# Optimization experiments

Hardware: AMD Instinct MI355X
Metric: run time of the kernel (lower is better)

Reference implementation:

```python
import jax, jax.numpy as jnp
import numpy as np

B, N, F_IN = 32, 512, 64
HEADS = (8, 8)
HIDS = (64, 64)
EDGE_P = 0.05  # graph density
NEG_SLOPE = 0.2
NEG_INF = -1e20


def setup_inputs() -> dict:
    key = jax.random.key(0)
    ks = jax.random.split(key, 8)
    x = jax.random.normal(ks[0], (B, N, F_IN), dtype=jnp.float32)
    adj = (jax.random.uniform(ks[1], (B, N, N)) < EDGE_P).astype(jnp.float32)
    adj = jnp.maximum(adj, adj.transpose(0, 2, 1))  # symmetric adjacency
    # mask = (batch, row): every (b, n) pair gets the masked softmax
    b_idx = jnp.repeat(jnp.arange(B, dtype=jnp.int32), N)   # [B*N]
    r_idx = jnp.tile(jnp.arange(N, dtype=jnp.int32), B)     # [B*N]
    # layer 0: f_in=64 -> f_out=64, H=8 ; layer 1: f_in=64*8=512 -> f_out=64, H=8
    W0 = jax.random.normal(ks[2], (F_IN, HIDS[0]), dtype=jnp.float32) / jnp.sqrt(jnp.float32(F_IN))
    a_src0 = jax.random.normal(ks[3], (HIDS[0], HEADS[0]), dtype=jnp.float32) / jnp.sqrt(jnp.float32(HIDS[0]))
    a_dst0 = jax.random.normal(ks[4], (HIDS[0], HEADS[0]), dtype=jnp.float32) / jnp.sqrt(jnp.float32(HIDS[0]))
    f_in1 = HIDS[0] * HEADS[0]
    W1 = jax.random.normal(ks[5], (f_in1, HIDS[1]), dtype=jnp.float32) / jnp.sqrt(jnp.float32(f_in1))
    a_src1 = jax.random.normal(ks[6], (HIDS[1], HEADS[1]), dtype=jnp.float32) / jnp.sqrt(jnp.float32(HIDS[1]))
    a_dst1 = jax.random.normal(ks[7], (HIDS[1], HEADS[1]), dtype=jnp.float32) / jnp.sqrt(jnp.float32(HIDS[1]))
    return dict(x=x, adj=adj, b_idx=b_idx, r_idx=r_idx,
                W0=W0, a_src0=a_src0, a_dst0=a_dst0,
                W1=W1, a_src1=a_src1, a_dst1=a_dst1)


def _gat_layer(x, adj, b_idx, r_idx, W, a_src, a_dst):
    # x: [B,N,f_in], adj: [B,N,N] (diag already set), W: [f_in,F], a_*: [F,H]
    hp = x @ W                                        # [B,N,F]
    s = jnp.einsum('bnf,fh->bhn', hp, a_src)          # attn_src
    d = jnp.einsum('bnf,fh->bhn', hp, a_dst)          # attn_dst
    attn = s[:, :, :, None] + d[:, :, None, :]        # [B,H,N,N]
    attn = jnp.where(attn >= 0, attn, NEG_SLOPE * attn)  # leaky_relu(0.2)
    attn = jnp.where(adj[:, None, :, :] == 0, 0.0, attn)  # masked_fill(adj==0, 0)
    rows = attn[b_idx, :, r_idx, :]                   # [K,H,N]
    rows = jnp.where(rows == 0.0, NEG_INF, rows)
    rows = jax.nn.softmax(rows, axis=-1)
    attn = attn.at[b_idx, :, r_idx, :].set(rows)
    return jnp.einsum('bhij,bjf->bhif', attn, hp)     # [B,H,N,F]


def reference(x, adj, b_idx, r_idx, W0, a_src0, a_dst0, W1, a_src1, a_dst1):
    Bn, Nn = x.shape[:2]
    # torch mutates adj in place: adj[batch,row,row] = 1 (self loops)
    adj = adj.at[b_idx, r_idx, r_idx].set(1.0)
    o = _gat_layer(x, adj, b_idx, r_idx, W0, a_src0, a_dst0)      # [B,H,N,F0]
    x1 = jax.nn.elu(o.transpose(0, 2, 1, 3).reshape(Bn, Nn, -1))  # [B,N,H*F0]
    o2 = _gat_layer(x1, adj, b_idx, r_idx, W1, a_src1, a_dst1)    # [B,H,N,F1]
    return o2.mean(axis=1)                                        # [B,N,F1]
```

## Files before the change

### kernel.cpp

```cpp
#include <hip/hip_runtime.h>
#include <hip/hip_bf16.h>
#include <math.h>

#define BB 32
#define NN 512

typedef _Float16 f16x8 __attribute__((ext_vector_type(8)));
typedef __fp16  fp16x2 __attribute__((ext_vector_type(2)));
typedef float f32x4 __attribute__((ext_vector_type(4)));

#define MFMA16(a, b, c) __builtin_amdgcn_mfma_f32_16x16x32_f16(a, b, c, 0, 0, 0)

union AF { f16x8 v; unsigned int u[4]; };

__device__ __forceinline__ void gload_lds16(const void* g, void* l) {
    __builtin_amdgcn_global_load_lds(
        (const __attribute__((address_space(1))) unsigned int*)g,
        (__attribute__((address_space(3))) unsigned int*)l, 16, 0, 0);
}

__global__ __launch_bounds__(256) void k_wt_prep(
    const float* __restrict__ W0, _Float16* __restrict__ W0T,
    const float* __restrict__ W1, _Float16* __restrict__ W1T)
{
    int id = blockIdx.x * 256 + threadIdx.x;
    const float* W; _Float16* WT; int KT, task;
    if (id < 512) { W = W0; WT = W0T; KT = 64;  task = id; }
    else          { W = W1; WT = W1T; KT = 512; task = id - 512; }
    int n = task & 63, gabs = task >> 6;
    int c = gabs >> 3, g = gabs & 7;
    f16x8 hv;
#pragma unroll
    for (int e = 0; e < 8; ++e)
        hv[e] = (_Float16)W[(size_t)(gabs * 8 + e) * 64 + n];
    *(f16x8*)(WT + (size_t)n * KT + c * 64 + (g ^ (n & 7)) * 8) = hv;
}

__global__ __launch_bounds__(256) void k_maxd(
    const float* __restrict__ dTg, float* __restrict__ maxd,
    float* __restrict__ E, float* __restrict__ Eb)
{
    __shared__ float sm[4];
    int bh = blockIdx.x;
    int t = threadIdx.x, lane = t & 63, w = t >> 6;
    const float* p = dTg + (size_t)bh * NN;
    float d0 = p[t], d1 = p[t + 256];
    float m = fmaxf(d0, d1);
#pragma unroll
    for (int off = 32; off; off >>= 1) m = fmaxf(m, __shfl_xor(m, off));
    if (lane == 0) sm[w] = m;
    __syncthreads();
    float mx = fmaxf(fmaxf(sm[0], sm[1]), fmaxf(sm[2], sm[3]));
    if (t == 0) maxd[bh] = mx;
    float* Ep  = E  + (size_t)bh * NN;
    float* Ebp = Eb + (size_t)bh * NN;
    Ep[t]        = __expf(d0 - mx);
    Ep[t + 256]  = __expf(d1 - mx);
    Ebp[t]       = __expf(0.2f * (d0 - mx));
    Ebp[t + 256] = __expf(0.2f * (d1 - mx));
}

static __device__ __forceinline__ void epi_sd_hpt(
    const float* ctile, const float* asd_f, int row0, int t,
    float* __restrict__ s, float* __restrict__ dTg, _Float16* __restrict__ hpT)
{
    int b = row0 >> 9, jb = row0 & 511;
    if (t < 128) {
        int rr = t >> 3, h = t & 7;
        float sv = 0.f, dv = 0.f;
#pragma unroll
        for (int f = 0; f < 64; ++f) {
            float hv = ctile[rr * 66 + f];
            sv = fmaf(hv, asd_f[f * 8 + h], sv);
            dv = fmaf(hv, asd_f[512 + f * 8 + h], dv);
        }
        s[((size_t)b * NN + jb + rr) * 8 + h] = sv;
        dTg[((size_t)b * 8 + h) * NN + jb + rr] = dv;
    } else {
        int t2 = t - 128;
        int f = t2 >> 1, jl = (t2 & 1) * 8;
        f16x8 hv;
#pragma unroll
        for (int e = 0; e < 8; ++e)
            hv[e] = (_Float16)ctile[(jl + e) * 66 + f];
        *(f16x8*)(hpT + ((size_t)b * 64 + f) * NN + jb + jl) = hv;
    }
}

__global__ __launch_bounds__(256) void k_gemm0(
    const float* __restrict__ x, const _Float16* __restrict__ W0T,
    const float* __restrict__ a_src, const float* __restrict__ a_dst,
    const float* __restrict__ adj, unsigned long long* __restrict__ adjb,
    float* __restrict__ s, float* __restrict__ dTg, _Float16* __restrict__ hpT)
{
    __shared__ float ctile[16 * 66];
    __shared__ float asd_f[1024];
    int t = threadIdx.x, row0 = blockIdx.x * 16;
    int lane = t & 63, w = t >> 6, cn = lane & 15, rq = lane >> 4;

    ((float4*)asd_f)[t] = (t < 128) ? ((const float4*)a_src)[t]
                                    : ((const float4*)a_dst)[t - 128];
    f32x4 acc;
#pragma unroll
    for (int e = 0; e < 4; ++e) acc[e] = 0.f;
#pragma unroll
    for (int ks = 0; ks < 2; ++ks) {
        const float* xp = x + (size_t)(row0 + cn) * 64 + ks * 32 + rq * 8;
        float4 x0 = *(const float4*)xp, x1 = *(const float4*)(xp + 4);
        f16x8 ah = {(_Float16)x0.x, (_Float16)x0.y, (_Float16)x0.z, (_Float16)x0.w,
                    (_Float16)x1.x, (_Float16)x1.y, (_Float16)x1.z, (_Float16)x1.w};
        int nn = w * 16 + cn;
        f16x8 bh = *(const f16x8*)(W0T + (size_t)nn * 64 + (((ks * 4 + rq) ^ (nn & 7)) * 8));
        acc = MFMA16(ah, bh, acc);
    }
#pragma unroll
    for (int r = 0; r < 4; ++r)
        ctile[(rq * 4 + r) * 66 + w * 16 + cn] = acc[r];
    __syncthreads();
    epi_sd_hpt(ctile, asd_f, row0, t, s, dTg, hpT);

#pragma unroll
    for (int rl = 0; rl < 4; ++rl) {
        int gi = row0 + w * 4 + rl;
        int i = gi & (NN - 1);
        const float* ap = adj + (size_t)gi * NN;
#pragma unroll
        for (int jc8 = 0; jc8 < 8; ++jc8) {
            float v = ap[jc8 * 64 + lane];
            unsigned long long m = __ballot((v != 0.f) || (jc8 * 64 + lane == i));
            if (lane == 0) adjb[(size_t)gi * 8 + jc8] = m;
        }
    }
}

template<int MODE>
__global__ __launch_bounds__(256, 4) void k_attn_fused(
    const unsigned long long* __restrict__ adjb, const float* __restrict__ s,
    const float* __restrict__ dTg, const float* __restrict__ maxd,
    const float* __restrict__ E, const float* __restrict__ Eb,
    const _Float16* __restrict__ hpT,
    const _Float16* __restrict__ W1T,
    const float* __restrict__ a_src, const float* __restrict__ a_dst,
    float* __restrict__ s_out, float* __restrict__ dTg_out,
    _Float16* __restrict__ hpT_out, float* __restrict__ o_f)
{
    __shared__ __align__(16) char smem[32768];
    _Float16* hTd0 = (_Float16*)smem;
    _Float16* hTd1 = (_Float16*)(smem + 8192);

    int blk = blockIdx.x;
    int vb = ((blk & 7) << 7) | (blk >> 3);
    int b = vb >> 5, i0 = (vb & 31) << 4;
    int row0 = vb * 16;
    int t = threadIdx.x, lane = t & 63, w = t >> 6;
    int cn = lane & 15, rq = lane >> 4;
    int h0 = 2 * w, h1 = h0 + 1;
    int myrow = i0 + cn;

    const _Float16* hb = hpT + (size_t)b * 64 * NN;

    int f0 = t >> 3, g0 = t & 7;
    const _Float16* src0 = hb + (size_t)f0 * NN + ((g0 ^ (f0 & 7)) * 8);
    const _Float16* src1 = hb + (size_t)(f0 + 32) * NN + ((g0 ^ (f0 & 7)) * 8);
    {
        _Float16* db = hTd0 + (w << 9);
        gload_lds16(src0, db);
        gload_lds16(src1, db + 2048);
    }

    float sv0 = s[((size_t)b * NN + myrow) * 8 + h0];
    float sv1 = s[((size_t)b * NN + myrow) * 8 + h1];
    float md0 = maxd[b * 8 + h0], md1 = maxd[b * 8 + h1];
    float M0 = fmaxf(sv0 + md0, 0.f);
    float M1 = fmaxf(sv1 + md1, 0.f);
    float c00 = __expf(sv0 + md0 - M0), cb0 = __expf(0.2f * (sv0 + md0) - M0);
    float c01 = __expf(sv1 + md1 - M1), cb1 = __expf(0.2f * (sv1 + md1) - M1);

    const float* dg0  = dTg + ((size_t)b * 8 + h0) * NN;
    const float* dg1  = dTg + ((size_t)b * 8 + h1) * NN;
    const float* Er0  = E   + ((size_t)b * 8 + h0) * NN;
    const float* Er1  = E   + ((size_t)b * 8 + h1) * NN;
    const float* Ebr0 = Eb  + ((size_t)b * 8 + h0) * NN;
    const float* Ebr1 = Eb  + ((size_t)b * 8 + h1) * NN;
    const unsigned long long* abr = adjb + ((size_t)b * NN + myrow) * 8;
    int rq8 = rq * 8;

    f16x8 ones;
#pragma unroll
    for (int e = 0; e < 8; ++e) ones[e] = (_Float16)1.0f;

    f32x4 acc[2][4], accrs[2];
#pragma unroll
    for (int hh = 0; hh < 2; ++hh) {
#pragma unroll
        for (int e = 0; e < 4; ++e) accrs[hh][e] = 0.f;
#pragma unroll
        for (int ft = 0; ft < 4; ++ft)
#pragma unroll
            for (int e = 0; e < 4; ++e) acc[hh][ft][e] = 0.f;
    }

    unsigned long long mb = abr[0];
    __syncthreads();

#pragma unroll 2
    for (int jcx = 0; jcx < 8; ++jcx) {
        int jc = jcx * 64;
        const _Float16* hTc = (jcx & 1) ? hTd1 : hTd0;
        if (jcx < 7) {
            _Float16* db = ((jcx & 1) ? hTd0 : hTd1) + (w << 9);
            gload_lds16(src0 + jc + 64, db);
            gload_lds16(src1 + jc + 64, db + 2048);
        }
        unsigned long long mbn = (jcx < 7) ? abr[jcx + 1] : 0ull;
        unsigned int ml = (unsigned int)mb, mhh = (unsigned int)(mb >> 32);
#pragma unroll
        for (int ks = 0; ks < 2; ++ks) {
            int j0 = jc + ks * 32 + rq8;
            unsigned int mby = ((ks ? mhh : ml) >> rq8) & 0xffu;
            float dd0[8], dd1[8], Ev0[8], Ev1[8], Eb0v[8], Eb1v[8];
            *(float4*)&dd0[0]  = *(const float4*)(dg0 + j0);
            *(float4*)&dd0[4]  = *(const float4*)(dg0 + j0 + 4);
            *(float4*)&dd1[0]  = *(const float4*)(dg1 + j0);
            *(float4*)&dd1[4]  = *(const float4*)(dg1 + j0 + 4);
            *(float4*)&Ev0[0]  = *(const float4*)(Er0 + j0);
            *(float4*)&Ev0[4]  = *(const float4*)(Er0 + j0 + 4);
            *(float4*)&Ev1[0]  = *(const float4*)(Er1 + j0);
            *(float4*)&Ev1[4]  = *(const float4*)(Er1 + j0 + 4);
            *(float4*)&Eb0v[0] = *(const float4*)(Ebr0 + j0);
            *(float4*)&Eb0v[4] = *(const float4*)(Ebr0 + j0 + 4);
            *(float4*)&Eb1v[0] = *(const float4*)(Ebr1 + j0);
            *(float4*)&Eb1v[4] = *(const float4*)(Ebr1 + j0 + 4);
            AF aA, aB;
#pragma unroll
            for (int e = 0; e < 8; e += 2) {
                float pA[2], pB[2];
#pragma unroll
                for (int q = 0; q < 2; ++q) {
                    int ee = e + q;
                    bool con = (mby >> ee) & 1u;
                    float e0 = sv0 + dd0[ee];
                    float p0 = (e0 >= 0.f) ? c00 * Ev0[ee] : cb0 * Eb0v[ee];
                    pA[q] = (con && e0 != 0.f) ? p0 : 0.f;
                    float e1 = sv1 + dd1[ee];
                    float p1 = (e1 >= 0.f) ? c01 * Ev1[ee] : cb1 * Eb1v[ee];
                    pB[q] = (con && e1 != 0.f) ? p1 : 0.f;
                }
                fp16x2 ka = __builtin_amdgcn_cvt_pkrtz(pA[0], pA[1]);
                fp16x2 kb = __builtin_amdgcn_cvt_pkrtz(pB[0], pB[1]);
                aA.u[e >> 1] = __builtin_bit_cast(unsigned int, ka);
                aB.u[e >> 1] = __builtin_bit_cast(unsigned int, kb);
            }
            accrs[0] = MFMA16(aA.v, ones, accrs[0]);
            accrs[1] = MFMA16(aB.v, ones, accrs[1]);
#pragma unroll
            for (int ft = 0; ft < 4; ++ft) {
                int f = ft * 16 + cn;
                f16x8 bh = *(const f16x8*)&hTc[f * 64 + (((ks * 4 + rq) ^ (f & 7)) * 8)];
                acc[0][ft] = MFMA16(aA.v, bh, acc[0][ft]);
                acc[1][ft] = MFMA16(aB.v, bh, acc[1][ft]);
            }
        }
        mb = mbn;
        __syncthreads();
    }

    float invr[2][4];
#pragma unroll
    for (int hh = 0; hh < 2; ++hh)
#pragma unroll
        for (int r = 0; r < 4; ++r) invr[hh][r] = 1.0f / accrs[hh][r];

    if (MODE == 0) {
        _Float16* Bst0 = (_Float16*)smem;
        _Float16* Bst1 = (_Float16*)(smem + 8192);
        const _Float16* wsrc = W1T + (size_t)(t >> 3) * 512 + ((t & 7) * 8);
        {
            _Float16* db = Bst0 + (w << 9);
            gload_lds16(wsrc, db);
            gload_lds16(wsrc + 32 * 512, db + 2048);
        }
        _Float16* x1all = (_Float16*)(smem + 16384);
#pragma unroll
        for (int hh = 0; hh < 2; ++hh) {
            int h = h0 + hh;
#pragma unroll
            for (int ft = 0; ft < 4; ++ft)
#pragma unroll
                for (int r = 0; r < 4; ++r) {
                    int il = rq * 4 + r;
                    float v = acc[hh][ft][r] * invr[hh][r];
                    v = v > 0.f ? v : __expf(v) - 1.f;
                    int f = ft * 16 + cn;
                    x1all[h * 1024 + il * 64 + (((f >> 3) ^ (il & 7)) * 8) + (f & 7)] =
                        (_Float16)v;
                }
        }
        __syncthreads();
        f32x4 g1;
#pragma unroll
        for (int e = 0; e < 4; ++e) g1[e] = 0.f;
        for (int kc = 0; kc < 8; ++kc) {
            const _Float16* Bc = (kc & 1) ? Bst1 : Bst0;
            if (kc < 7) {
                _Float16* db = ((kc & 1) ? Bst0 : Bst1) + (w << 9);
                gload_lds16(wsrc + (kc + 1) * 64, db);
                gload_lds16(wsrc + 32 * 512 + (kc + 1) * 64, db + 2048);
            }
#pragma unroll
            for (int ks = 0; ks < 2; ++ks) {
                int pa = (((ks * 4 + rq) ^ (cn & 7)) * 8);
                f16x8 ah = *(const f16x8*)&x1all[kc * 1024 + cn * 64 + pa];
                int nn = w * 16 + cn;
                f16x8 bh = *(const f16x8*)&Bc[nn * 64 + (((ks * 4 + rq) ^ (nn & 7)) * 8)];
                g1 = MFMA16(ah, bh, g1);
            }
            __syncthreads();
        }
        float* ctile = (float*)(smem + 16384);
        float* asd_f = (float*)(smem + 24576);
#pragma unroll
        for (int r = 0; r < 4; ++r)
            ctile[(rq * 4 + r) * 66 + w * 16 + cn] = g1[r];
        ((float4*)asd_f)[t] = (t < 128) ? ((const float4*)a_src)[t]
                                        : ((const float4*)a_dst)[t - 128];
        __syncthreads();
        epi_sd_hpt(ctile, asd_f, row0, t, s_out, dTg_out, hpT_out);
    } else {
        float* red = (float*)smem;
#pragma unroll
        for (int ft = 0; ft < 4; ++ft)
#pragma unroll
            for (int r = 0; r < 4; ++r) {
                int il = rq * 4 + r;
                float v = acc[0][ft][r] * invr[0][r]
                        + acc[1][ft][r] * invr[1][r];
                red[(w * 16 + il) * 64 + ft * 16 + cn] = v;
            }
        __syncthreads();
#pragma unroll
        for (int u = 0; u < 4; ++u) {
            int idx = t + u * 256;
            int il = idx >> 6, f = idx & 63;
            float sum = red[il * 64 + f] + red[(16 + il) * 64 + f]
                      + red[(32 + il) * 64 + f] + red[(48 + il) * 64 + f];
            o_f[((size_t)b * NN + i0 + il) * 64 + f] = sum * 0.125f;
        }
    }
}

extern "C" void kernel_launch(void* const* d_in, const int* in_sizes, int n_in,
                              void* d_out, int out_size, void* d_ws, size_t ws_size,
                              hipStream_t stream) {
    const float* x      = (const float*)d_in[0];
    const float* adj    = (const float*)d_in[1];
    const float* W0     = (const float*)d_in[4];
    const float* a_src0 = (const float*)d_in[5];
    const float* a_dst0 = (const float*)d_in[6];
    const float* W1     = (const float*)d_in[7];
    const float* a_src1 = (const float*)d_in[8];
    const float* a_dst1 = (const float*)d_in[9];
    float* out = (float*)d_out;

    float* ws = (float*)d_ws;
    const size_t R = (size_t)BB * NN;
    const size_t BHN = (size_t)BB * 8 * NN;
    float* s0    = ws;
    float* dTg0  = s0 + R * 8;
    float* s1    = dTg0 + BHN;
    float* dTg1  = s1 + R * 8;
    float* maxd0 = dTg1 + BHN;
    float* maxd1 = maxd0 + 256;
    float* E0    = maxd1 + 256;
    float* Eb0   = E0 + BHN;
    float* E1    = Eb0 + BHN;
    float* Eb1   = E1 + BHN;
    _Float16* hp0T = (_Float16*)(Eb1 + BHN);
    _Float16* hp1T = hp0T + (size_t)BB * 64 * NN;
    _Float16* W0T  = hp1T + (size_t)BB * 64 * NN;
    _Float16* W1T  = W0T + (size_t)64 * 64;
    unsigned long long* adjb = (unsigned long long*)(W1T + (size_t)64 * 512);

    k_wt_prep<<<18, 256, 0, stream>>>(W0, W0T, W1, W1T);
    k_gemm0<<<1024, 256, 0, stream>>>(x, W0T, a_src0, a_dst0, adj, adjb,
                                      s0, dTg0, hp0T);
    k_maxd<<<256, 256, 0, stream>>>(dTg0, maxd0, E0, Eb0);
    k_attn_fused<0><<<1024, 256, 0, stream>>>(adjb, s0, dTg0, maxd0, E0, Eb0,
                                              hp0T, W1T, a_src1, a_dst1,
                                              s1, dTg1, hp1T, nullptr);
    k_maxd<<<256, 256, 0, stream>>>(dTg1, maxd1, E1, Eb1);
    k_attn_fused<1><<<1024, 256, 0, stream>>>(adjb, s1, dTg1, maxd1, E1, Eb1,
                                              hp1T, nullptr, nullptr, nullptr,
                                              nullptr, nullptr, nullptr, out);
}
```

Measured before the change: 187.8 us.

## Compute attention exponentials inline, prefetch dst scores, vectorize adjacency bitmask build

Drops the precomputed E/Eb exponential tables. k_maxd now writes only the per-(batch,head) max, and the attention kernel computes exp(leaky(s+d)-M) directly in the inner loop. The dst-score loads are software-pipelined with double buffers across the two k-steps of each tile. k_gemm0 now builds the adjacency bitmask from coalesced float4 loads issued early, packed through shared memory, replacing per-row ballots. The aim is to cut global traffic and load latency in the attention loop, in exchange for more transcendental ALU work per element.

```diff
diff --git a/kernel.cpp b/kernel.cpp
--- a/kernel.cpp
+++ b/kernel.cpp
@@ -37,27 +37,18 @@
 }
 
 __global__ __launch_bounds__(256) void k_maxd(
-    const float* __restrict__ dTg, float* __restrict__ maxd,
-    float* __restrict__ E, float* __restrict__ Eb)
+    const float* __restrict__ dTg, float* __restrict__ maxd)
 {
     __shared__ float sm[4];
     int bh = blockIdx.x;
     int t = threadIdx.x, lane = t & 63, w = t >> 6;
     const float* p = dTg + (size_t)bh * NN;
-    float d0 = p[t], d1 = p[t + 256];
-    float m = fmaxf(d0, d1);
+    float m = fmaxf(p[t], p[t + 256]);
 #pragma unroll
     for (int off = 32; off; off >>= 1) m = fmaxf(m, __shfl_xor(m, off));
     if (lane == 0) sm[w] = m;
     __syncthreads();
-    float mx = fmaxf(fmaxf(sm[0], sm[1]), fmaxf(sm[2], sm[3]));
-    if (t == 0) maxd[bh] = mx;
-    float* Ep  = E  + (size_t)bh * NN;
-    float* Ebp = Eb + (size_t)bh * NN;
-    Ep[t]        = __expf(d0 - mx);
-    Ep[t + 256]  = __expf(d1 - mx);
-    Ebp[t]       = __expf(0.2f * (d0 - mx));
-    Ebp[t + 256] = __expf(0.2f * (d1 - mx));
+    if (t == 0) maxd[bh] = fmaxf(fmaxf(sm[0], sm[1]), fmaxf(sm[2], sm[3]));
 }
 
 static __device__ __forceinline__ void epi_sd_hpt(
@@ -95,8 +86,15 @@
 {
     __shared__ float ctile[16 * 66];
     __shared__ float asd_f[1024];
+    __shared__ unsigned int mrow[16][16];
     int t = threadIdx.x, row0 = blockIdx.x * 16;
     int lane = t & 63, w = t >> 6, cn = lane & 15, rq = lane >> 4;
+
+    int ar = t >> 4, seg = t & 15;
+    const float* ap = adj + (size_t)(row0 + ar) * NN + seg * 32;
+    float4 av[8];
+#pragma unroll
+    for (int q = 0; q < 8; ++q) av[q] = ((const float4*)ap)[q];
 
     ((float4*)asd_f)[t] = (t < 128) ? ((const float4*)a_src)[t]
                                     : ((const float4*)a_dst)[t - 128];
@@ -119,25 +117,73 @@
     __syncthreads();
     epi_sd_hpt(ctile, asd_f, row0, t, s, dTg, hpT);
 
-#pragma unroll
-    for (int rl = 0; rl < 4; ++rl) {
-        int gi = row0 + w * 4 + rl;
-        int i = gi & (NN - 1);
-        const float* ap = adj + (size_t)gi * NN;
-#pragma unroll
-        for (int jc8 = 0; jc8 < 8; ++jc8) {
-            float v = ap[jc8 * 64 + lane];
-            unsigned long long m = __ballot((v != 0.f) || (jc8 * 64 + lane == i));
-            if (lane == 0) adjb[(size_t)gi * 8 + jc8] = m;
-        }
-    }
-}
+    unsigned int m32 = 0;
+#pragma unroll
+    for (int q = 0; q < 8; ++q) {
+        if (av[q].x != 0.f) m32 |= 1u << (q * 4 + 0);
+        if (av[q].y != 0.f) m32 |= 1u << (q * 4 + 1);
+        if (av[q].z != 0.f) m32 |= 1u << (q * 4 + 2);
+        if (av[q].w != 0.f) m32 |= 1u << (q * 4 + 3);
+    }
+    int i = (row0 + ar) & (NN - 1);
+    if ((i >> 5) == seg) m32 |= 1u << (i & 31);
+    mrow[ar][seg] = m32;
+    __syncthreads();
+    if (t < 128) {
+        int r = t >> 3, k = t & 7;
+        unsigned long long u = (unsigned long long)mrow[r][2 * k]
+                             | ((unsigned long long)mrow[r][2 * k + 1] << 32);
+        adjb[(size_t)(row0 + r) * 8 + k] = u;
+    }
+}
+
+#define LD8(DST0, DST1, J)                                              \
+    do {                                                                \
+        *(float4*)&DST0[0] = *(const float4*)(dg0 + (J));               \
+        *(float4*)&DST0[4] = *(const float4*)(dg0 + (J) + 4);           \
+        *(float4*)&DST1[0] = *(const float4*)(dg1 + (J));               \
+        *(float4*)&DST1[4] = *(const float4*)(dg1 + (J) + 4);           \
+    } while (0)
+
+#define PSTEP(DD0v, DD1v, MBYTE, KS, HTC)                               \
+    do {                                                                \
+        AF aA, aB;                                                      \
+        _Pragma("unroll")                                               \
+        for (int e = 0; e < 8; e += 2) {                                \
+            float pA[2], pB[2];                                         \
+            _Pragma("unroll")                                           \
+            for (int q = 0; q < 2; ++q) {                               \
+                int ee = e + q;                                         \
+                bool con = (MBYTE >> ee) & 1u;                          \
+                float e0 = sv0 + DD0v[ee];                              \
+                float l0 = fmaxf(e0, 0.2f * e0);                        \
+                float p0 = __expf(l0 - M0);                             \
+                pA[q] = (con && l0 != 0.f) ? p0 : 0.f;                  \
+                float e1 = sv1 + DD1v[ee];                              \
+                float l1 = fmaxf(e1, 0.2f * e1);                        \
+                float p1 = __expf(l1 - M1);                             \
+                pB[q] = (con && l1 != 0.f) ? p1 : 0.f;                  \
+            }                                                           \
+            fp16x2 ka = __builtin_amdgcn_cvt_pkrtz(pA[0], pA[1]);       \
+            fp16x2 kb = __builtin_amdgcn_cvt_pkrtz(pB[0], pB[1]);       \
+            aA.u[e >> 1] = __builtin_bit_cast(unsigned int, ka);        \
+            aB.u[e >> 1] = __builtin_bit_cast(unsigned int, kb);        \
+        }                                                               \
+        accrs[0] = MFMA16(aA.v, ones, accrs[0]);                        \
+        accrs[1] = MFMA16(aB.v, ones, accrs[1]);                        \
+        _Pragma("unroll")                                               \
+        for (int ft = 0; ft < 4; ++ft) {                                \
+            int f = ft * 16 + cn;                                       \
+            f16x8 bh = *(const f16x8*)&HTC[f * 64 + ((((KS) * 4 + rq) ^ (f & 7)) * 8)]; \
+            acc[0][ft] = MFMA16(aA.v, bh, acc[0][ft]);                  \
+            acc[1][ft] = MFMA16(aB.v, bh, acc[1][ft]);                  \
+        }                                                               \
+    } while (0)
 
 template<int MODE>
 __global__ __launch_bounds__(256, 4) void k_attn_fused(
     const unsigned long long* __restrict__ adjb, const float* __restrict__ s,
     const float* __restrict__ dTg, const float* __restrict__ maxd,
-    const float* __restrict__ E, const float* __restrict__ Eb,
     const _Float16* __restrict__ hpT,
     const _Float16* __restrict__ W1T,
     const float* __restrict__ a_src, const float* __restrict__ a_dst,
@@ -170,18 +216,11 @@
 
     float sv0 = s[((size_t)b * NN + myrow) * 8 + h0];
     float sv1 = s[((size_t)b * NN + myrow) * 8 + h1];
-    float md0 = maxd[b * 8 + h0], md1 = maxd[b * 8 + h1];
-    float M0 = fmaxf(sv0 + md0, 0.f);
-    float M1 = fmaxf(sv1 + md1, 0.f);
-    float c00 = __expf(sv0 + md0 - M0), cb0 = __expf(0.2f * (sv0 + md0) - M0);
-    float c01 = __expf(sv1 + md1 - M1), cb1 = __expf(0.2f * (sv1 + md1) - M1);
-
-    const float* dg0  = dTg + ((size_t)b * 8 + h0) * NN;
-    const float* dg1  = dTg + ((size_t)b * 8 + h1) * NN;
-    const float* Er0  = E   + ((size_t)b * 8 + h0) * NN;
-    const float* Er1  = E   + ((size_t)b * 8 + h1) * NN;
-    const float* Ebr0 = Eb  + ((size_t)b * 8 + h0) * NN;
-    const float* Ebr1 = Eb  + ((size_t)b * 8 + h1) * NN;
+    float M0 = fmaxf(sv0 + maxd[b * 8 + h0], 0.f);
+    float M1 = fmaxf(sv1 + maxd[b * 8 + h1], 0.f);
+
+    const float* dg0 = dTg + ((size_t)b * 8 + h0) * NN;
+    const float* dg1 = dTg + ((size_t)b * 8 + h1) * NN;
     const unsigned long long* abr = adjb + ((size_t)b * NN + myrow) * 8;
     int rq8 = rq * 8;
 
@@ -200,10 +239,11 @@
             for (int e = 0; e < 4; ++e) acc[hh][ft][e] = 0.f;
     }
 
+    float ddA0[8], ddA1[8], ddB0[8], ddB1[8];
     unsigned long long mb = abr[0];
+    LD8(ddA0, ddA1, rq8);
     __syncthreads();
 
-#pragma unroll 2
     for (int jcx = 0; jcx < 8; ++jcx) {
         int jc = jcx * 64;
         const _Float16* hTc = (jcx & 1) ? hTd1 : hTd0;
@@ -214,52 +254,15 @@
         }
         unsigned long long mbn = (jcx < 7) ? abr[jcx + 1] : 0ull;
         unsigned int ml = (unsigned int)mb, mhh = (unsigned int)(mb >> 32);
-#pragma unroll
-        for (int ks = 0; ks < 2; ++ks) {
-            int j0 = jc + ks * 32 + rq8;
-            unsigned int mby = ((ks ? mhh : ml) >> rq8) & 0xffu;
-            float dd0[8], dd1[8], Ev0[8], Ev1[8], Eb0v[8], Eb1v[8];
-            *(float4*)&dd0[0]  = *(const float4*)(dg0 + j0);
-            *(float4*)&dd0[4]  = *(const float4*)(dg0 + j0 + 4);
-            *(float4*)&dd1[0]  = *(const float4*)(dg1 + j0);
-            *(float4*)&dd1[4]  = *(const float4*)(dg1 + j0 + 4);
-            *(float4*)&Ev0[0]  = *(const float4*)(Er0 + j0);
-            *(float4*)&Ev0[4]  = *(const float4*)(Er0 + j0 + 4);
-            *(float4*)&Ev1[0]  = *(const float4*)(Er1 + j0);
-            *(float4*)&Ev1[4]  = *(const float4*)(Er1 + j0 + 4);
-            *(float4*)&Eb0v[0] = *(const float4*)(Ebr0 + j0);
-            *(float4*)&Eb0v[4] = *(const float4*)(Ebr0 + j0 + 4);
-            *(float4*)&Eb1v[0] = *(const float4*)(Ebr1 + j0);
-            *(float4*)&Eb1v[4] = *(const float4*)(Ebr1 + j0 + 4);
-            AF aA, aB;
-#pragma unroll
-            for (int e = 0; e < 8; e += 2) {
-                float pA[2], pB[2];
-#pragma unroll
-                for (int q = 0; q < 2; ++q) {
-                    int ee = e + q;
-                    bool con = (mby >> ee) & 1u;
-                    float e0 = sv0 + dd0[ee];
-                    float p0 = (e0 >= 0.f) ? c00 * Ev0[ee] : cb0 * Eb0v[ee];
-                    pA[q] = (con && e0 != 0.f) ? p0 : 0.f;
-                    float e1 = sv1 + dd1[ee];
-                    float p1 = (e1 >= 0.f) ? c01 * Ev1[ee] : cb1 * Eb1v[ee];
-                    pB[q] = (con && e1 != 0.f) ? p1 : 0.f;
-                }
-                fp16x2 ka = __builtin_amdgcn_cvt_pkrtz(pA[0], pA[1]);
-                fp16x2 kb = __builtin_amdgcn_cvt_pkrtz(pB[0], pB[1]);
-                aA.u[e >> 1] = __builtin_bit_cast(unsigned int, ka);
-                aB.u[e >> 1] = __builtin_bit_cast(unsigned int, kb);
-            }
-            accrs[0] = MFMA16(aA.v, ones, accrs[0]);
-            accrs[1] = MFMA16(aB.v, ones, accrs[1]);
-#pragma unroll
-            for (int ft = 0; ft < 4; ++ft) {
-                int f = ft * 16 + cn;
-                f16x8 bh = *(const f16x8*)&hTc[f * 64 + (((ks * 4 + rq) ^ (f & 7)) * 8)];
-                acc[0][ft] = MFMA16(aA.v, bh, acc[0][ft]);
-                acc[1][ft] = MFMA16(aB.v, bh, acc[1][ft]);
-            }
+        LD8(ddB0, ddB1, jc + 32 + rq8);
+        {
+            unsigned int mby = (ml >> rq8) & 0xffu;
+            PSTEP(ddA0, ddA1, mby, 0, hTc);
+        }
+        if (jcx < 7) LD8(ddA0, ddA1, jc + 64 + rq8);
+        {
+            unsigned int mby = (mhh >> rq8) & 0xffu;
+            PSTEP(ddB0, ddB1, mby, 1, hTc);
         }
         mb = mbn;
         __syncthreads();
@@ -371,11 +374,7 @@
     float* dTg1  = s1 + R * 8;
     float* maxd0 = dTg1 + BHN;
     float* maxd1 = maxd0 + 256;
-    float* E0    = maxd1 + 256;
-    float* Eb0   = E0 + BHN;
-    float* E1    = Eb0 + BHN;
-    float* Eb1   = E1 + BHN;
-    _Float16* hp0T = (_Float16*)(Eb1 + BHN);
+    _Float16* hp0T = (_Float16*)(maxd1 + 256);
     _Float16* hp1T = hp0T + (size_t)BB * 64 * NN;
     _Float16* W0T  = hp1T + (size_t)BB * 64 * NN;
     _Float16* W1T  = W0T + (size_t)64 * 64;
@@ -384,12 +383,12 @@
     k_wt_prep<<<18, 256, 0, stream>>>(W0, W0T, W1, W1T);
     k_gemm0<<<1024, 256, 0, stream>>>(x, W0T, a_src0, a_dst0, adj, adjb,
                                       s0, dTg0, hp0T);
-    k_maxd<<<256, 256, 0, stream>>>(dTg0, maxd0, E0, Eb0);
-    k_attn_fused<0><<<1024, 256, 0, stream>>>(adjb, s0, dTg0, maxd0, E0, Eb0,
-                                              hp0T, W1T, a_src1, a_dst1,
+    k_maxd<<<256, 256, 0, stream>>>(dTg0, maxd0);
+    k_attn_fused<0><<<1024, 256, 0, stream>>>(adjb, s0, dTg0, maxd0, hp0T,
+                                              W1T, a_src1, a_dst1,
                                               s1, dTg1, hp1T, nullptr);
-    k_maxd<<<256, 256, 0, stream>>>(dTg1, maxd1, E1, Eb1);
-    k_attn_fused<1><<<1024, 256, 0, stream>>>(adjb, s1, dTg1, maxd1, E1, Eb1,
-                                              hp1T, nullptr, nullptr, nullptr,
+    k_maxd<<<256, 256, 0, stream>>>(dTg1, maxd1);
+    k_attn_fused<1><<<1024, 256, 0, stream>>>(adjb, s1, dTg1, maxd1, hp1T,
+                                              nullptr, nullptr, nullptr,
                                               nullptr, nullptr, nullptr, out);
 }
```

After: 159.7 us. -15.0%, faster.
